# Performance work log

Hardware: AMD Instinct MI355X
Metric: run time of the kernel (lower is better)

The kernel has to match this reference:

```python
import jax, jax.numpy as jnp
import numpy as np
import math

PHI = (1.0 + math.sqrt(5.0)) / 2.0
B, S, E, H = 4, 1024, 1024, 16
D = E // H  # head_dim = 64


def setup_inputs() -> dict:
    key = jax.random.key(0)
    ks = jax.random.split(key, 16)
    w = 0.02  # stand-in for xavier(gain=1/phi); math is init-agnostic
    inp = {
        "query": jax.random.normal(ks[0], (B, S, E), jnp.float32),
        "key": jax.random.normal(ks[1], (B, S, E), jnp.float32),
        "value": jax.random.normal(ks[2], (B, S, E), jnp.float32),
        "consciousness_levels": jax.random.uniform(ks[3], (B, S), jnp.float32),
        # causal mask, broadcast over batch and heads
        "attn_mask": jnp.tril(jnp.ones((S, S), bool))[None, None],
        # projection weights stored [in, out] (torch Linear applies x @ W.T)
        "Wq": jax.random.normal(ks[4], (E, E), jnp.float32) * w,
        "bq": jnp.zeros((E,), jnp.float32),
        "Wk": jax.random.normal(ks[5], (E, E), jnp.float32) * w,
        "bk": jnp.zeros((E,), jnp.float32),
        "Wv": jax.random.normal(ks[6], (E, E), jnp.float32) * w,
        "bv": jnp.zeros((E,), jnp.float32),
        "Wo": jax.random.normal(ks[7], (E, E), jnp.float32) * w,
        "bo": jnp.zeros((E,), jnp.float32),
        "Wc": jax.random.normal(ks[8], (E, H), jnp.float32) * w,
        "bc": jnp.zeros((H,), jnp.float32),
        # phi_bias[h] = (h+1)/phi**(h+1), shape [H,1,1] as in _init_weights
        "phi_bias": jnp.array([(h + 1) / PHI ** (h + 1) for h in range(H)],
                               jnp.float32).reshape(H, 1, 1),
    }
    return inp


def reference(query, key, value, consciousness_levels, attn_mask,
              Wq, bq, Wk, bk, Wv, bv, Wo, bo, Wc, bc, phi_bias):
    # project and split heads: [B,S,E] -> [B,H,S,D]
    q = (query @ Wq + bq).reshape(B, S, H, D).transpose(0, 2, 1, 3)
    k = (key @ Wk + bk).reshape(B, S, H, D).transpose(0, 2, 1, 3)
    v = (value @ Wv + bv).reshape(B, S, H, D).transpose(0, 2, 1, 3)

    inv_scale = 1.0 / (math.sqrt(D) * math.sqrt(PHI))  # phi-scaled 1/sqrt(d)
    scores = jnp.einsum('bhqd,bhkd->bhqk', q, k) * inv_scale
    scores = scores + phi_bias[None]                   # per-head additive bias
    scores = jnp.where(attn_mask, scores, -jnp.inf)
    attn = jax.nn.softmax(scores, axis=-1)             # [B,H,S,S]

    # consciousness reweighting + second softmax (faithful to original)
    cw = jax.nn.softmax(query @ Wc + bc, axis=-1)      # [B,S,H]
    cw = cw.transpose(0, 2, 1)[..., None]              # [B,H,S,1]
    cb = consciousness_levels[:, None, :, None]        # [B,1,S,1]
    attn = jax.nn.softmax(attn * (1.0 + cb * cw), axis=-1)

    ctx = jnp.einsum('bhqk,bhkd->bhqd', attn, v)
    ctx = ctx.transpose(0, 2, 1, 3).reshape(B, S, E)
    out = ctx @ Wo + bo
    return out, attn
```

## Files before the change

### kernel.cpp

```cpp
#include <hip/hip_runtime.h>
#include <stdint.h>

#define B_ 4
#define S_ 1024
#define E_ 1024
#define H_ 16
#define D_ 64

typedef unsigned short u16;
typedef short s16x8 __attribute__((ext_vector_type(8)));
typedef unsigned short u16x8 __attribute__((ext_vector_type(8)));
typedef unsigned short u16x4 __attribute__((ext_vector_type(4)));
typedef unsigned short u16x2 __attribute__((ext_vector_type(2)));
typedef float f32x4 __attribute__((ext_vector_type(4)));

__device__ __forceinline__ u16 f2bf(float f) {
    union { float f; uint32_t i; } x; x.f = f;
    uint32_t r = (x.i + 0x7FFFu + ((x.i >> 16) & 1u)) >> 16;
    return (u16)r;
}

__device__ __forceinline__ float wave_sum(float v) {
    #pragma unroll
    for (int o = 32; o; o >>= 1) v += __shfl_xor(v, o);
    return v;
}

__device__ __forceinline__ void gload16(const u16* g, u16* l) {
    __builtin_amdgcn_global_load_lds(
        (const __attribute__((address_space(1))) void*)g,
        (__attribute__((address_space(3))) void*)l, 16, 0, 0);
}

template<int BM, int BN>
__device__ __forceinline__ void gemm_core(
    const u16* __restrict__ Ab, int lda,
    const u16* __restrict__ Bp, int ldb,
    int m0, int n0, int K,
    u16* As, u16* Bs, f32x4 (&acc)[BM / 32][BN / 32])
{
    constexpr int FM = BM / 32, FN = BN / 32;
    constexpr int ACH = BM / 64;
    constexpr int BCH = BN / 64;
    const int t = threadIdx.x, lane = t & 63, w = t >> 6;
    const int wr = w >> 1, wc = w & 1, al = lane & 15, aq = lane >> 4;

    auto stage = [&](int buf, int k0) {
        u16* Ad = As + buf * (BM * 32);
        u16* Bd = Bs + buf * (BN * 32);
        #pragma unroll
        for (int i = 0; i < ACH; i++) {
            const int c = i * 256 + w * 64 + lane;
            gload16(Ab + (size_t)(m0 + (c >> 2)) * lda + k0 + (c & 3) * 8,
                    Ad + (size_t)(i * 256 + w * 64) * 8);
        }
        #pragma unroll
        for (int i = 0; i < BCH; i++) {
            const int c = i * 256 + w * 64 + lane;
            gload16(Bp + (size_t)(n0 + (c >> 2)) * ldb + k0 + (c & 3) * 8,
                    Bd + (size_t)(i * 256 + w * 64) * 8);
        }
    };
    auto compute = [&](int buf) {
        const u16* Ar = As + buf * (BM * 32);
        const u16* Br = Bs + buf * (BN * 32);
        s16x8 af[FM], bf[FN];
        #pragma unroll
        for (int i = 0; i < FM; i++)
            af[i] = *(const s16x8*)(Ar + ((wr * FM + i) * 16 + al) * 32 + aq * 8);
        #pragma unroll
        for (int j = 0; j < FN; j++)
            bf[j] = *(const s16x8*)(Br + ((wc * FN + j) * 16 + al) * 32 + aq * 8);
        #pragma unroll
        for (int i = 0; i < FM; i++)
            #pragma unroll
            for (int j = 0; j < FN; j++)
                acc[i][j] = __builtin_amdgcn_mfma_f32_16x16x32_bf16(af[i], bf[j], acc[i][j], 0, 0, 0);
    };

    int cur = 0;
    stage(0, 0);
    for (int k0 = 32; k0 < K; k0 += 32) {
        asm volatile("s_waitcnt vmcnt(0)" ::: "memory");
        __syncthreads();
        stage(cur ^ 1, k0);
        compute(cur);
        cur ^= 1;
    }
    asm volatile("s_waitcnt vmcnt(0)" ::: "memory");
    __syncthreads();
    compute(cur);
}

__global__ __launch_bounds__(256, 3)
void gemm_qkv(const u16* __restrict__ qbf, const u16* __restrict__ kbf,
              const u16* __restrict__ vbf, const u16* __restrict__ wt,
              const float* __restrict__ bq, const float* __restrict__ bk,
              const float* __restrict__ bv,
              u16* __restrict__ q_ws, u16* __restrict__ k_ws,
              u16* __restrict__ vt_ws)
{
    __shared__ __attribute__((aligned(16))) u16 As[2 * 128 * 32];
    __shared__ __attribute__((aligned(16))) u16 Bs[2 * 128 * 32];
    const int flat = blockIdx.x + (blockIdx.y << 3) + (blockIdx.z << 8);
    const int z = flat >> 8;
    const int y = flat & 31;
    const int x = (flat >> 5) & 7;
    const u16* Ab = (z == 0) ? qbf : (z == 1) ? kbf : vbf;
    const u16* Bp = wt + (size_t)z * E_ * E_;
    const float* bias = (z == 0) ? bq : (z == 1) ? bk : bv;
    u16* Cb = (z == 0) ? q_ws : (z == 1) ? k_ws : vt_ws;
    const int m0 = y * 128, n0 = x * 128;

    f32x4 acc[4][4];
    #pragma unroll
    for (int i = 0; i < 4; i++)
        #pragma unroll
        for (int j = 0; j < 4; j++)
            acc[i][j] = (f32x4){0.f, 0.f, 0.f, 0.f};

    gemm_core<128, 128>(Ab, E_, Bp, E_, m0, n0, E_, As, Bs, acc);

    const int t = threadIdx.x, lane = t & 63, w = t >> 6;
    const int wr = w >> 1, wc = w & 1, al = lane & 15, aq = lane >> 4;
    #pragma unroll
    for (int i = 0; i < 4; i++) {
        #pragma unroll
        for (int j = 0; j < 4; j++) {
            const int col = n0 + (wc * 4 + j) * 16 + al;
            const float bvv = bias[col];
            #pragma unroll
            for (int r = 0; r < 4; r++) {
                const int row = m0 + (wr * 4 + i) * 16 + aq * 4 + r;
                const float vv = acc[i][j][r] + bvv;
                const int b = row >> 10, s = row & 1023, h = col >> 6, d = col & 63;
                if (z < 2)
                    Cb[((size_t)((b * H_ + h) * S_ + s)) * D_ + d] = f2bf(vv);
                else
                    Cb[((size_t)((b * H_ + h) * D_ + d)) * S_ + s] = f2bf(vv);
            }
        }
    }
}

__global__ __launch_bounds__(256, 3)
void gemm_o(const u16* __restrict__ ctx, const u16* __restrict__ wt3,
            const float* __restrict__ bo, float* __restrict__ out)
{
    __shared__ __attribute__((aligned(16))) u16 As[2 * 128 * 32];
    __shared__ __attribute__((aligned(16))) u16 Bs[2 * 64 * 32];
    const int flat = blockIdx.x + (blockIdx.y << 4);
    const int y = flat & 31;
    const int x = flat >> 5;
    const int m0 = y * 128, n0 = x * 64;

    f32x4 acc[4][2];
    #pragma unroll
    for (int i = 0; i < 4; i++)
        #pragma unroll
        for (int j = 0; j < 2; j++)
            acc[i][j] = (f32x4){0.f, 0.f, 0.f, 0.f};

    gemm_core<128, 64>(ctx, E_, wt3, E_, m0, n0, E_, As, Bs, acc);

    const int t = threadIdx.x, lane = t & 63, w = t >> 6;
    const int wr = w >> 1, wc = w & 1, al = lane & 15, aq = lane >> 4;
    #pragma unroll
    for (int i = 0; i < 4; i++) {
        #pragma unroll
        for (int j = 0; j < 2; j++) {
            const int col = n0 + (wc * 2 + j) * 16 + al;
            const float bvv = bo[col];
            #pragma unroll
            for (int r = 0; r < 4; r++) {
                const int row = m0 + (wr * 4 + i) * 16 + aq * 4 + r;
                __builtin_nontemporal_store(acc[i][j][r] + bvv,
                                            &out[(size_t)row * E_ + col]);
            }
        }
    }
}

__global__ __launch_bounds__(256)
void prelude_k(const float* __restrict__ query, const float* __restrict__ key_,
               const float* __restrict__ value,
               const float* __restrict__ Wq, const float* __restrict__ Wk,
               const float* __restrict__ Wv, const float* __restrict__ Wo,
               const float* __restrict__ Wc, const float* __restrict__ bc,
               const float* __restrict__ cl,
               u16* __restrict__ qbf, u16* __restrict__ kbf,
               u16* __restrict__ vbf, u16* __restrict__ wt,
               float* __restrict__ mws)
{
    __shared__ float tile[64][65];
    const int bid = blockIdx.x, t = threadIdx.x;

    if (bid < 512) {
        const int tid = bid * 256 + t;
        #pragma unroll
        for (int j = 0; j < 4; j++) {
            const int i = tid + j * 131072;
            {
                f32x4 a = *(const f32x4*)(query + (size_t)i * 8);
                f32x4 b = *(const f32x4*)(query + (size_t)i * 8 + 4);
                u16x8 o;
                o[0] = f2bf(a[0]); o[1] = f2bf(a[1]); o[2] = f2bf(a[2]); o[3] = f2bf(a[3]);
                o[4] = f2bf(b[0]); o[5] = f2bf(b[1]); o[6] = f2bf(b[2]); o[7] = f2bf(b[3]);
                *(u16x8*)(qbf + (size_t)i * 8) = o;
            }
            {
                f32x4 a = *(const f32x4*)(key_ + (size_t)i * 8);
                f32x4 b = *(const f32x4*)(key_ + (size_t)i * 8 + 4);
                u16x8 o;
                o[0] = f2bf(a[0]); o[1] = f2bf(a[1]); o[2] = f2bf(a[2]); o[3] = f2bf(a[3]);
                o[4] = f2bf(b[0]); o[5] = f2bf(b[1]); o[6] = f2bf(b[2]); o[7] = f2bf(b[3]);
                *(u16x8*)(kbf + (size_t)i * 8) = o;
            }
            {
                f32x4 a = *(const f32x4*)(value + (size_t)i * 8);
                f32x4 b = *(const f32x4*)(value + (size_t)i * 8 + 4);
                u16x8 o;
                o[0] = f2bf(a[0]); o[1] = f2bf(a[1]); o[2] = f2bf(a[2]); o[3] = f2bf(a[3]);
                o[4] = f2bf(b[0]); o[5] = f2bf(b[1]); o[6] = f2bf(b[2]); o[7] = f2bf(b[3]);
                *(u16x8*)(vbf + (size_t)i * 8) = o;
            }
        }
    } else if (bid < 1536) {
        const int tb = bid - 512;
        const int zz = tb >> 8, rem = tb & 255;
        const int by = (rem >> 4) * 64, bx = (rem & 15) * 64;
        const float* in = (zz == 0) ? Wq : (zz == 1) ? Wk : (zz == 2) ? Wv : Wo;
        u16* o = wt + (size_t)zz * E_ * E_;
        const int tx = t & 63, ty = t >> 6;
        #pragma unroll
        for (int i = 0; i < 16; i++) {
            const int r = ty + i * 4;
            tile[r][tx] = in[(size_t)(by + r) * E_ + bx + tx];
        }
        __syncthreads();
        #pragma unroll
        for (int i = 0; i < 16; i++) {
            const int r = ty + i * 4;
            o[(size_t)(bx + r) * E_ + by + tx] = f2bf(tile[tx][r]);
        }
    } else {
        const int lane = t & 63, wave = t >> 6;
        const int r = (bid - 1536) * 4 + wave;
        const float* qrow = query + (size_t)r * E_;
        float acc[H_];
        #pragma unroll
        for (int c = 0; c < H_; c++) acc[c] = 0.f;
        for (int e = lane; e < E_; e += 64) {
            float qv = qrow[e];
            const float* wp = Wc + e * H_;
            f32x4 w0 = *(const f32x4*)(wp);
            f32x4 w1 = *(const f32x4*)(wp + 4);
            f32x4 w2 = *(const f32x4*)(wp + 8);
            f32x4 w3 = *(const f32x4*)(wp + 12);
            #pragma unroll
            for (int c = 0; c < 4; c++) {
                acc[c]      += qv * w0[c];
                acc[4 + c]  += qv * w1[c];
                acc[8 + c]  += qv * w2[c];
                acc[12 + c] += qv * w3[c];
            }
        }
        #pragma unroll
        for (int c = 0; c < H_; c++) acc[c] = wave_sum(acc[c]);
        float mx = -3e38f;
        #pragma unroll
        for (int c = 0; c < H_; c++) { acc[c] += bc[c]; mx = fmaxf(mx, acc[c]); }
        float se = 0.f;
        #pragma unroll
        for (int c = 0; c < H_; c++) { acc[c] = __expf(acc[c] - mx); se += acc[c]; }
        if (lane < H_) {
            float mycw = 0.f;
            #pragma unroll
            for (int c = 0; c < H_; c++) if (lane == c) mycw = acc[c];
            mycw /= se;
            int b = r >> 10, s = r & 1023;
            float clv = cl[r];
            mws[((size_t)(b * H_ + lane)) * S_ + s] = 1.f + clv * mycw;
        }
    }
}

#define LDS_ 1028
__global__ __launch_bounds__(512, 4)
void attn_fused(const u16* __restrict__ q_ws, const u16* __restrict__ k_ws,
                const u16* __restrict__ vt_ws, const float* __restrict__ mws,
                float* __restrict__ attn_out, u16* __restrict__ ctx_ws,
                float alpha)
{
    __shared__ __attribute__((aligned(16))) float Sf[16 * LDS_];
    float* dmp = Sf;
    __shared__ float red[8 * 16];
    __shared__ float sclA[16], invzA[16];

    const int t = threadIdx.x, lane = t & 63, w = t >> 6;
    const int al = lane & 15, aq = lane >> 4;
    const int bh = blockIdx.x;
    const int q0 = blockIdx.y << 4;

    const u16* Qp = q_ws + ((size_t)bh * S_ + q0) * D_;
    const u16* Kp = k_ws + ((size_t)bh * S_ + w * 128) * D_;
    const u16* Vp = vt_ws + (size_t)bh * D_ * S_;

    s16x8 qb0 = *(const s16x8*)(Qp + (size_t)al * D_ + aq * 8);
    s16x8 qb1 = *(const s16x8*)(Qp + (size_t)al * D_ + 32 + aq * 8);
    const int qg = q0 + al;
    f32x4 ee[8];
    float s1 = 0.f;
    #pragma unroll
    for (int mf = 0; mf < 8; mf++) {
        const u16* kr = Kp + (size_t)(mf * 16 + al) * D_ + aq * 8;
        s16x8 ka0 = *(const s16x8*)(kr);
        s16x8 ka1 = *(const s16x8*)(kr + 32);
        f32x4 a0 = (f32x4){0.f, 0.f, 0.f, 0.f};
        a0 = __builtin_amdgcn_mfma_f32_16x16x32_bf16(ka0, qb0, a0, 0, 0, 0);
        a0 = __builtin_amdgcn_mfma_f32_16x16x32_bf16(ka1, qb1, a0, 0, 0, 0);
        const int k0i = w * 128 + mf * 16 + aq * 4;
        #pragma unroll
        for (int r = 0; r < 4; r++) {
            float e = (k0i + r <= qg) ? __expf(a0[r] * alpha) : 0.f;
            ee[mf][r] = e;
            s1 += e;
        }
    }
    s1 += __shfl_xor(s1, 16);
    s1 += __shfl_xor(s1, 32);
    if (lane < 16) red[w * 16 + al] = s1;
    __syncthreads();
    if (t < 16) {
        float s = 0.f;
        #pragma unroll
        for (int c = 0; c < 8; c++) s += red[c * 16 + t];
        sclA[t] = mws[(size_t)bh * S_ + q0 + t] / s;
    }
    __syncthreads();

    const float sl = sclA[al];
    float s2 = 0.f;
    #pragma unroll
    for (int mf = 0; mf < 8; mf++) {
        const int k0i = w * 128 + mf * 16 + aq * 4;
        #pragma unroll
        for (int r = 0; r < 4; r++) {
            float e = (k0i + r <= qg) ? __expf(ee[mf][r] * sl) : 1.f;
            ee[mf][r] = e;
            s2 += e;
        }
    }
    s2 += __shfl_xor(s2, 16);
    s2 += __shfl_xor(s2, 32);
    if (lane < 16) red[w * 16 + al] = s2;
    __syncthreads();
    if (t < 16) {
        float s = 0.f;
        #pragma unroll
        for (int c = 0; c < 8; c++) s += red[c * 16 + t];
        invzA[t] = 1.f / s;
    }
    #pragma unroll
    for (int mf = 0; mf < 8; mf++) {
        const int k0i = w * 128 + mf * 16 + aq * 4;
        *(f32x4*)(Sf + (size_t)al * LDS_ + k0i) = ee[mf];
    }
    __syncthreads();

    float* ao = attn_out + (size_t)bh * S_ * S_ + (size_t)q0 * S_;
    #pragma unroll
    for (int rr = 0; rr < 2; rr++) {
        const int r2 = w * 2 + rr;
        const float iz = invzA[r2];
        #pragma unroll
        for (int k2 = 0; k2 < 4; k2++) {
            f32x4 v = *(const f32x4*)(Sf + (size_t)r2 * LDS_ + k2 * 256 + lane * 4);
            f32x4 o;
            #pragma unroll
            for (int j = 0; j < 4; j++) o[j] = v[j] * iz;
            __builtin_nontemporal_store(o, (f32x4*)(ao + (size_t)r2 * S_ + k2 * 256 + lane * 4));
        }
    }

    f32x4 pa[4];
    #pragma unroll
    for (int nf = 0; nf < 4; nf++) pa[nf] = (f32x4){0.f, 0.f, 0.f, 0.f};
    #pragma unroll
    for (int ks = 0; ks < 4; ks++) {
        const int kb = w * 128 + ks * 32;
        const float* ap = Sf + (size_t)al * LDS_ + kb + aq * 8;
        f32x4 x0 = *(const f32x4*)(ap);
        f32x4 x1 = *(const f32x4*)(ap + 4);
        s16x8 af;
        af[0] = (short)f2bf(x0[0]); af[1] = (short)f2bf(x0[1]);
        af[2] = (short)f2bf(x0[2]); af[3] = (short)f2bf(x0[3]);
        af[4] = (short)f2bf(x1[0]); af[5] = (short)f2bf(x1[1]);
        af[6] = (short)f2bf(x1[2]); af[7] = (short)f2bf(x1[3]);
        #pragma unroll
        for (int nf = 0; nf < 4; nf++) {
            s16x8 bv = *(const s16x8*)(Vp + (size_t)(nf * 16 + al) * S_ + kb + aq * 8);
            pa[nf] = __builtin_amdgcn_mfma_f32_16x16x32_bf16(af, bv, pa[nf], 0, 0, 0);
        }
    }
    __syncthreads();

    {
        float* dp = dmp + w * (64 * 20);
        #pragma unroll
        for (int nf = 0; nf < 4; nf++)
            *(f32x4*)(dp + (size_t)(nf * 16 + al) * 20 + aq * 4) = pa[nf];
    }
    __syncthreads();
    {
        const int r5 = t >> 5, d0 = (t & 31) * 2;
        const float iz = invzA[r5];
        float o0 = 0.f, o1 = 0.f;
        #pragma unroll
        for (int ww = 0; ww < 8; ww++) {
            const float* rp5 = dmp + ww * (64 * 20) + r5;
            o0 += rp5[(size_t)d0 * 20];
            o1 += rp5[(size_t)(d0 + 1) * 20];
        }
        const int b = bh >> 4, h = bh & 15;
        u16* cp = ctx_ws + ((size_t)(b * S_ + q0 + r5)) * E_ + h * 64 + d0;
        u16x2 ob;
        ob[0] = f2bf(o0 * iz);
        ob[1] = f2bf(o1 * iz);
        *(u16x2*)cp = ob;
    }
}

extern "C" void kernel_launch(void* const* d_in, const int* in_sizes, int n_in,
                              void* d_out, int out_size, void* d_ws, size_t ws_size,
                              hipStream_t stream)
{
    const float* query = (const float*)d_in[0];
    const float* key_  = (const float*)d_in[1];
    const float* value = (const float*)d_in[2];
    const float* cl    = (const float*)d_in[3];
    const float* Wq = (const float*)d_in[5];
    const float* bq = (const float*)d_in[6];
    const float* Wk = (const float*)d_in[7];
    const float* bk = (const float*)d_in[8];
    const float* Wv = (const float*)d_in[9];
    const float* bv = (const float*)d_in[10];
    const float* Wo = (const float*)d_in[11];
    const float* bo = (const float*)d_in[12];
    const float* Wc = (const float*)d_in[13];
    const float* bc = (const float*)d_in[14];

    float* out  = (float*)d_out;
    float* attn = out + (size_t)B_ * S_ * E_;

    u16* q_ws   = (u16*)d_ws;
    u16* k_ws   = q_ws  + (size_t)B_ * S_ * E_;
    u16* vt_ws  = k_ws  + (size_t)B_ * S_ * E_;
    u16* ctx_ws = vt_ws + (size_t)B_ * S_ * E_;
    u16* wt     = ctx_ws + (size_t)B_ * S_ * E_;
    float* mws  = (float*)(wt + (size_t)4 * E_ * E_);

    u16* qbf = (u16*)attn;
    u16* kbf = qbf + (size_t)B_ * S_ * E_;
    u16* vbf = kbf + (size_t)B_ * S_ * E_;

    const float inv_scale = 0.09826892502579689f;
    dim3 blk(256);

    prelude_k<<<2560, blk, 0, stream>>>(query, key_, value, Wq, Wk, Wv, Wo,
                                        Wc, bc, cl, qbf, kbf, vbf, wt, mws);

    gemm_qkv<<<dim3(8, 32, 3), blk, 0, stream>>>(
        qbf, kbf, vbf, wt, bq, bk, bv, q_ws, k_ws, vt_ws);

    attn_fused<<<dim3(B_ * H_, S_ / 16), dim3(512), 0, stream>>>(
        q_ws, k_ws, vt_ws, mws, attn, ctx_ws, inv_scale);

    gemm_o<<<dim3(16, 32, 1), blk, 0, stream>>>(
        ctx_ws, wt + (size_t)3 * E_ * E_, bo, out);
}
```

Before: 535.9 us.

## Skip masked causal tiles by rewriting second softmax as exp-minus-one plus V column sum

Rewrites the second softmax so masked positions, each exp(0)=1, are handled analytically. Stored values become exp(x)-1, which is zero when masked, the normaliser adds S, and the constant term becomes a precomputed per-head column sum of V from a new small kernel. This lets each wave skip QK^T MFMAs and PV MFMAs for key tiles entirely beyond the causal limit, cutting roughly half the attention compute. It adds an extra launch, and the exp-minus-one with bf16 conversion of P may shift numerics slightly.

Result: faster. 510.0 us (-4.8%).

```diff
diff --git a/kernel.cpp b/kernel.cpp
--- a/kernel.cpp
+++ b/kernel.cpp
@@ -18,6 +18,11 @@
     union { float f; uint32_t i; } x; x.f = f;
     uint32_t r = (x.i + 0x7FFFu + ((x.i >> 16) & 1u)) >> 16;
     return (u16)r;
+}
+
+__device__ __forceinline__ float bf2f(u16 u) {
+    union { uint32_t i; float f; } x; x.i = ((uint32_t)u) << 16;
+    return x.f;
 }
 
 __device__ __forceinline__ float wave_sum(float v) {
@@ -285,10 +290,32 @@
     }
 }
 
+__global__ __launch_bounds__(256)
+void vsum_k(const u16* __restrict__ vt_ws, float* __restrict__ vsum)
+{
+    const int bh = blockIdx.x;
+    const int t = threadIdx.x, lane = t & 63, ww = t >> 6;
+    #pragma unroll
+    for (int dd = 0; dd < 16; dd++) {
+        const int d = ww * 16 + dd;
+        const u16* row = vt_ws + ((size_t)bh * D_ + d) * S_;
+        float s = 0.f;
+        #pragma unroll
+        for (int c = 0; c < 2; c++) {
+            u16x8 v = *(const u16x8*)(row + (size_t)(c * 64 + lane) * 8);
+            #pragma unroll
+            for (int j = 0; j < 8; j++) s += bf2f(v[j]);
+        }
+        s = wave_sum(s);
+        if (lane == 0) vsum[bh * D_ + d] = s;
+    }
+}
+
 #define LDS_ 1028
 __global__ __launch_bounds__(512, 4)
 void attn_fused(const u16* __restrict__ q_ws, const u16* __restrict__ k_ws,
                 const u16* __restrict__ vt_ws, const float* __restrict__ mws,
+                const float* __restrict__ vsum,
                 float* __restrict__ attn_out, u16* __restrict__ ctx_ws,
                 float alpha)
 {
@@ -305,6 +332,10 @@
     const u16* Qp = q_ws + ((size_t)bh * S_ + q0) * D_;
     const u16* Kp = k_ws + ((size_t)bh * S_ + w * 128) * D_;
     const u16* Vp = vt_ws + (size_t)bh * D_ * S_;
+
+    const int lim = q0 + 15 - w * 128;
+    const int nmf = (lim < 0) ? 0 : ((lim >> 4) + 1 > 8 ? 8 : (lim >> 4) + 1);
+    const int nks = (lim < 0) ? 0 : ((lim >> 5) + 1 > 4 ? 4 : (lim >> 5) + 1);
 
     s16x8 qb0 = *(const s16x8*)(Qp + (size_t)al * D_ + aq * 8);
     s16x8 qb1 = *(const s16x8*)(Qp + (size_t)al * D_ + 32 + aq * 8);
@@ -313,18 +344,20 @@
     float s1 = 0.f;
     #pragma unroll
     for (int mf = 0; mf < 8; mf++) {
-        const u16* kr = Kp + (size_t)(mf * 16 + al) * D_ + aq * 8;
-        s16x8 ka0 = *(const s16x8*)(kr);
-        s16x8 ka1 = *(const s16x8*)(kr + 32);
-        f32x4 a0 = (f32x4){0.f, 0.f, 0.f, 0.f};
-        a0 = __builtin_amdgcn_mfma_f32_16x16x32_bf16(ka0, qb0, a0, 0, 0, 0);
-        a0 = __builtin_amdgcn_mfma_f32_16x16x32_bf16(ka1, qb1, a0, 0, 0, 0);
-        const int k0i = w * 128 + mf * 16 + aq * 4;
-        #pragma unroll
-        for (int r = 0; r < 4; r++) {
-            float e = (k0i + r <= qg) ? __expf(a0[r] * alpha) : 0.f;
-            ee[mf][r] = e;
-            s1 += e;
+        if (mf < nmf) {
+            const u16* kr = Kp + (size_t)(mf * 16 + al) * D_ + aq * 8;
+            s16x8 ka0 = *(const s16x8*)(kr);
+            s16x8 ka1 = *(const s16x8*)(kr + 32);
+            f32x4 a0 = (f32x4){0.f, 0.f, 0.f, 0.f};
+            a0 = __builtin_amdgcn_mfma_f32_16x16x32_bf16(ka0, qb0, a0, 0, 0, 0);
+            a0 = __builtin_amdgcn_mfma_f32_16x16x32_bf16(ka1, qb1, a0, 0, 0, 0);
+            const int k0i = w * 128 + mf * 16 + aq * 4;
+            #pragma unroll
+            for (int r = 0; r < 4; r++) {
+                float e = (k0i + r <= qg) ? __expf(a0[r] * alpha) : 0.f;
+                ee[mf][r] = e;
+                s1 += e;
+            }
         }
     }
     s1 += __shfl_xor(s1, 16);
@@ -344,12 +377,18 @@
     #pragma unroll
     for (int mf = 0; mf < 8; mf++) {
         const int k0i = w * 128 + mf * 16 + aq * 4;
-        #pragma unroll
-        for (int r = 0; r < 4; r++) {
-            float e = (k0i + r <= qg) ? __expf(ee[mf][r] * sl) : 1.f;
-            ee[mf][r] = e;
-            s2 += e;
-        }
+        f32x4 o4;
+        if (mf < nmf) {
+            #pragma unroll
+            for (int r = 0; r < 4; r++) {
+                float e = (k0i + r <= qg) ? (__expf(ee[mf][r] * sl) - 1.f) : 0.f;
+                o4[r] = e;
+                s2 += e;
+            }
+        } else {
+            o4 = (f32x4){0.f, 0.f, 0.f, 0.f};
+        }
+        *(f32x4*)(Sf + (size_t)al * LDS_ + k0i) = o4;
     }
     s2 += __shfl_xor(s2, 16);
     s2 += __shfl_xor(s2, 32);
@@ -359,12 +398,7 @@
         float s = 0.f;
         #pragma unroll
         for (int c = 0; c < 8; c++) s += red[c * 16 + t];
-        invzA[t] = 1.f / s;
-    }
-    #pragma unroll
-    for (int mf = 0; mf < 8; mf++) {
-        const int k0i = w * 128 + mf * 16 + aq * 4;
-        *(f32x4*)(Sf + (size_t)al * LDS_ + k0i) = ee[mf];
+        invzA[t] = 1.f / (s + (float)S_);
     }
     __syncthreads();
 
@@ -378,7 +412,7 @@
             f32x4 v = *(const f32x4*)(Sf + (size_t)r2 * LDS_ + k2 * 256 + lane * 4);
             f32x4 o;
             #pragma unroll
-            for (int j = 0; j < 4; j++) o[j] = v[j] * iz;
+            for (int j = 0; j < 4; j++) o[j] = (v[j] + 1.f) * iz;
             __builtin_nontemporal_store(o, (f32x4*)(ao + (size_t)r2 * S_ + k2 * 256 + lane * 4));
         }
     }
@@ -388,19 +422,21 @@
     for (int nf = 0; nf < 4; nf++) pa[nf] = (f32x4){0.f, 0.f, 0.f, 0.f};
     #pragma unroll
     for (int ks = 0; ks < 4; ks++) {
-        const int kb = w * 128 + ks * 32;
-        const float* ap = Sf + (size_t)al * LDS_ + kb + aq * 8;
-        f32x4 x0 = *(const f32x4*)(ap);
-        f32x4 x1 = *(const f32x4*)(ap + 4);
-        s16x8 af;
-        af[0] = (short)f2bf(x0[0]); af[1] = (short)f2bf(x0[1]);
-        af[2] = (short)f2bf(x0[2]); af[3] = (short)f2bf(x0[3]);
-        af[4] = (short)f2bf(x1[0]); af[5] = (short)f2bf(x1[1]);
-        af[6] = (short)f2bf(x1[2]); af[7] = (short)f2bf(x1[3]);
-        #pragma unroll
-        for (int nf = 0; nf < 4; nf++) {
-            s16x8 bv = *(const s16x8*)(Vp + (size_t)(nf * 16 + al) * S_ + kb + aq * 8);
-            pa[nf] = __builtin_amdgcn_mfma_f32_16x16x32_bf16(af, bv, pa[nf], 0, 0, 0);
+        if (ks < nks) {
+            const int kb = w * 128 + ks * 32;
+            const float* ap = Sf + (size_t)al * LDS_ + kb + aq * 8;
+            f32x4 x0 = *(const f32x4*)(ap);
+            f32x4 x1 = *(const f32x4*)(ap + 4);
+            s16x8 af;
+            af[0] = (short)f2bf(x0[0]); af[1] = (short)f2bf(x0[1]);
+            af[2] = (short)f2bf(x0[2]); af[3] = (short)f2bf(x0[3]);
+            af[4] = (short)f2bf(x1[0]); af[5] = (short)f2bf(x1[1]);
+            af[6] = (short)f2bf(x1[2]); af[7] = (short)f2bf(x1[3]);
+            #pragma unroll
+            for (int nf = 0; nf < 4; nf++) {
+                s16x8 bv = *(const s16x8*)(Vp + (size_t)(nf * 16 + al) * S_ + kb + aq * 8);
+                pa[nf] = __builtin_amdgcn_mfma_f32_16x16x32_bf16(af, bv, pa[nf], 0, 0, 0);
+            }
         }
     }
     __syncthreads();
@@ -422,6 +458,8 @@
             o0 += rp5[(size_t)d0 * 20];
             o1 += rp5[(size_t)(d0 + 1) * 20];
         }
+        o0 += vsum[bh * D_ + d0];
+        o1 += vsum[bh * D_ + d0 + 1];
         const int b = bh >> 4, h = bh & 15;
         u16* cp = ctx_ws + ((size_t)(b * S_ + q0 + r5)) * E_ + h * 64 + d0;
         u16x2 ob;
@@ -459,6 +497,7 @@
     u16* ctx_ws = vt_ws + (size_t)B_ * S_ * E_;
     u16* wt     = ctx_ws + (size_t)B_ * S_ * E_;
     float* mws  = (float*)(wt + (size_t)4 * E_ * E_);
+    float* vsum = mws + (size_t)B_ * H_ * S_;
 
     u16* qbf = (u16*)attn;
     u16* kbf = qbf + (size_t)B_ * S_ * E_;
@@ -473,8 +512,10 @@
     gemm_qkv<<<dim3(8, 32, 3), blk, 0, stream>>>(
         qbf, kbf, vbf, wt, bq, bk, bv, q_ws, k_ws, vt_ws);
 
+    vsum_k<<<B_ * H_, blk, 0, stream>>>(vt_ws, vsum);
+
     attn_fused<<<dim3(B_ * H_, S_ / 16), dim3(512), 0, stream>>>(
-        q_ws, k_ws, vt_ws, mws, attn, ctx_ws, inv_scale);
+        q_ws, k_ws, vt_ws, mws, vsum, attn, ctx_ws, inv_scale);
 
     gemm_o<<<dim3(16, 32, 1), blk, 0, stream>>>(
         ctx_ws, wt + (size_t)3 * E_ * E_, bo, out);
```
